# Performance work log

Hardware: AMD Instinct MI355X
Metric: run time of the kernel (lower is better)

The kernel has to match this reference:

```python
import jax, jax.numpy as jnp
import numpy as np

NX = 1024
N_HEAD = 16
B = 2
N = 2048


def setup_inputs() -> dict:
    key = jax.random.key(0)
    k1, k2, k3 = jax.random.split(key, 3)
    x = jax.random.normal(k1, (B, N, NX), dtype=jnp.float32)
    # masked_fill mask: True where attention is NOT allowed (above diagonal)
    mask_self_attention = ~jnp.tril(jnp.ones((N, N), dtype=bool))[None, None]
    c_attn_w = jax.random.normal(k2, (NX, 3 * NX), dtype=jnp.float32) * 0.02
    c_attn_b = jnp.zeros((3 * NX,), dtype=jnp.float32)
    c_proj_w = jax.random.normal(k3, (NX, NX), dtype=jnp.float32) * 0.02
    c_proj_b = jnp.zeros((NX,), dtype=jnp.float32)
    return {
        'x': x,
        'c_attn_w': c_attn_w,
        'c_attn_b': c_attn_b,
        'c_proj_w': c_proj_w,
        'c_proj_b': c_proj_b,
        'mask_self_attention': mask_self_attention,
    }


def reference(x, c_attn_w, c_attn_b, c_proj_w, c_proj_b, mask_self_attention):
    hd = NX // N_HEAD  # head dim = 64
    qkv = x @ c_attn_w + c_attn_b                      # [B,N,3*NX]
    q, k, v = jnp.split(qkv, 3, axis=-1)
    # split heads -> [B,H,N,hd]
    q = q.reshape(B, N, N_HEAD, hd).transpose(0, 2, 1, 3)
    v = v.reshape(B, N, N_HEAD, hd).transpose(0, 2, 1, 3)
    k_t = k.reshape(B, N, N_HEAD, hd).transpose(0, 2, 3, 1)  # [B,H,hd,N]
    present = jnp.stack((k_t.transpose(0, 1, 3, 2), v))      # [2,B,H,N,hd]
    w = jnp.einsum('bhqd,bhdk->bhqk', q, k_t)
    w = w / jnp.sqrt(jnp.float32(hd))  # scale=True
    w = jnp.where(mask_self_attention, jnp.float32(-10000.0), w)
    w = jax.nn.softmax(w, axis=-1)
    a = jnp.einsum('bhqk,bhkd->bhqd', w, v)            # [B,H,N,hd]
    a = a.transpose(0, 2, 1, 3).reshape(B, N, NX)      # merge heads
    a = a @ c_proj_w + c_proj_b
    return (a, present)
```

## Files before the change

kernel.cpp:

```cpp
#include <hip/hip_runtime.h>
#include <cstddef>
#include <cstdint>

#define NX_ 1024
#define NH_ 16
#define HD_ 64
#define B_  2
#define N_  2048
#define M_  (B_ * N_)

typedef __attribute__((ext_vector_type(8))) short bf16x8;
typedef __attribute__((ext_vector_type(4))) float f32x4;

__device__ __forceinline__ unsigned short f2bf(float f) {
    union { float f; unsigned u; } v; v.f = f;
    return (unsigned short)((v.u + 0x7FFFu + ((v.u >> 16) & 1u)) >> 16);
}
__device__ __forceinline__ unsigned pk2bf(float a, float b) {
    return (unsigned)f2bf(a) | ((unsigned)f2bf(b) << 16);
}
__device__ __forceinline__ int szf(int r) { return (r & 3) ^ ((r >> 2) & 3); }

template<int NOUT, int MODE>
__global__ __launch_bounds__(256, 2)
void gemm_mfma(const float* __restrict__ Af, const unsigned short* __restrict__ Ah,
               const float* __restrict__ W, const float* __restrict__ bias,
               float* __restrict__ o_pk, float* __restrict__ o_pv,
               unsigned short* __restrict__ o_q, unsigned short* __restrict__ o_k,
               unsigned short* __restrict__ o_vt, float* __restrict__ o_f)
{
    __shared__ __align__(16) unsigned short As[2][128 * 32];
    __shared__ __align__(16) unsigned short Bs[2][128 * 32];
    const int t = threadIdx.x;
    const int l = t & 63;
    const int g = l >> 4, q15 = l & 15;
    const int w = t >> 6, wm = w >> 1, wn = w & 1;
    const int m0 = blockIdx.y * 128, j0 = blockIdx.x * 128;

    f32x4 acc[4][4];
#pragma unroll
    for (int i = 0; i < 4; i++)
#pragma unroll
        for (int j = 0; j < 4; j++) { acc[i][j][0]=0.f; acc[i][j][1]=0.f; acc[i][j][2]=0.f; acc[i][j][3]=0.f; }

    const int ra = t >> 1, ca = (t & 1) * 16;
    const int nb = t & 127, kb0 = (t >> 7) * 16;

    unsigned sa[8], sb[8];

#define LOAD_A(K0)                                                              \
    do {                                                                        \
        if (MODE == 0) {                                                        \
            const float* ap = Af + (size_t)(m0 + ra) * 1024 + (K0) + ca;        \
            float4 x0 = *(const float4*)(ap);                                   \
            float4 x1 = *(const float4*)(ap + 4);                               \
            float4 x2 = *(const float4*)(ap + 8);                               \
            float4 x3 = *(const float4*)(ap + 12);                              \
            sa[0] = pk2bf(x0.x, x0.y); sa[1] = pk2bf(x0.z, x0.w);               \
            sa[2] = pk2bf(x1.x, x1.y); sa[3] = pk2bf(x1.z, x1.w);               \
            sa[4] = pk2bf(x2.x, x2.y); sa[5] = pk2bf(x2.z, x2.w);               \
            sa[6] = pk2bf(x3.x, x3.y); sa[7] = pk2bf(x3.z, x3.w);               \
        } else {                                                                \
            const uint4* ap = (const uint4*)(Ah + (size_t)(m0 + ra) * 1024 + (K0) + ca); \
            uint4 u0 = ap[0], u1 = ap[1];                                       \
            sa[0]=u0.x; sa[1]=u0.y; sa[2]=u0.z; sa[3]=u0.w;                     \
            sa[4]=u1.x; sa[5]=u1.y; sa[6]=u1.z; sa[7]=u1.w;                     \
        }                                                                       \
    } while (0)

#define LOAD_B(K0)                                                              \
    do {                                                                        \
        const float* wp = W + (size_t)((K0) + kb0) * NOUT + j0 + nb;            \
        float v0,v1;                                                            \
        _Pragma("unroll")                                                       \
        for (int i = 0; i < 8; i++) {                                           \
            v0 = wp[(size_t)(2*i) * NOUT]; v1 = wp[(size_t)(2*i+1) * NOUT];     \
            sb[i] = pk2bf(v0, v1);                                              \
        }                                                                       \
    } while (0)

#define COMMIT_AB(BUF)                                                          \
    do {                                                                        \
        unsigned short* da = &As[BUF][ra * 32];                                 \
        const int s0a = (ca >> 3);                                              \
        *(uint4*)&da[((s0a ^ szf(ra)) & 3) * 8]       = *(uint4*)&sa[0];        \
        *(uint4*)&da[(((s0a + 1) ^ szf(ra)) & 3) * 8] = *(uint4*)&sa[4];        \
        unsigned short* db = &Bs[BUF][nb * 32];                                 \
        const int s0b = (kb0 >> 3);                                             \
        *(uint4*)&db[((s0b ^ szf(nb)) & 3) * 8]       = *(uint4*)&sb[0];        \
        *(uint4*)&db[(((s0b + 1) ^ szf(nb)) & 3) * 8] = *(uint4*)&sb[4];        \
    } while (0)

    LOAD_A(0); LOAD_B(0); COMMIT_AB(0);
    __syncthreads();

    for (int k0 = 0; k0 < 1024; k0 += 32) {
        const int buf = (k0 >> 5) & 1;
        const bool more = (k0 + 32 < 1024);
        if (more) { LOAD_A(k0 + 32); LOAD_B(k0 + 32); }

        bf16x8 af[4], bf[4];
#pragma unroll
        for (int mt = 0; mt < 4; mt++) {
            const int m = wm * 64 + mt * 16 + q15;
            af[mt] = *(const bf16x8*)&As[buf][m * 32 + ((g ^ szf(m)) & 3) * 8];
        }
#pragma unroll
        for (int nt = 0; nt < 4; nt++) {
            const int n = wn * 64 + nt * 16 + q15;
            bf[nt] = *(const bf16x8*)&Bs[buf][n * 32 + ((g ^ szf(n)) & 3) * 8];
        }
#pragma unroll
        for (int mt = 0; mt < 4; mt++)
#pragma unroll
            for (int nt = 0; nt < 4; nt++)
                acc[mt][nt] = __builtin_amdgcn_mfma_f32_16x16x32_bf16(af[mt], bf[nt], acc[mt][nt], 0, 0, 0);

        if (more) COMMIT_AB(buf ^ 1);
        __syncthreads();
    }

#pragma unroll
    for (int nt = 0; nt < 4; nt++) {
        const int ncol = wn * 64 + nt * 16 + q15;
        const int jc = j0 + ncol;
        const float bz = bias[jc];
        const int sec = jc >> 10, jl = jc & 1023, hh = jl >> 6, dd = jl & 63;
#pragma unroll
        for (int mt = 0; mt < 4; mt++) {
#pragma unroll
            for (int r = 0; r < 4; r++) {
                const int m = m0 + wm * 64 + mt * 16 + g * 4 + r;
                const float val = acc[mt][nt][r] + bz;
                if (MODE == 1) {
                    o_f[(size_t)m * NOUT + jc] = val;
                } else {
                    const int bb = m >> 11, nn = m & 2047;
                    const int bhh = bb * NH_ + hh;
                    const size_t idx = ((size_t)bhh * N_ + nn) * HD_ + dd;
                    if (sec == 0)      o_q[idx] = f2bf(val * 0.18033688f);
                    else if (sec == 1) { o_pk[idx] = val; o_k[idx] = f2bf(val); }
                    else               { o_pv[idx] = val;
                                         o_vt[((size_t)bhh * HD_ + dd) * N_ + nn] = f2bf(val); }
                }
            }
        }
    }
#undef LOAD_A
#undef LOAD_B
#undef COMMIT_AB
}

__global__ __launch_bounds__(256, 4)
void attn_mfma(const unsigned short* __restrict__ q_bf,
               const unsigned short* __restrict__ k_bf,
               const unsigned short* __restrict__ v_t,
               unsigned short* __restrict__ a_pre)
{
    __shared__ __align__(16) unsigned short Ks[2][64 * 64];
    __shared__ __align__(16) unsigned short Vt[2][64 * 64];
    __shared__ __align__(16) unsigned short Ps[64 * 64];

    const int t = threadIdx.x, l = t & 63, w = t >> 6;
    const int g = l >> 4, q15 = l & 15;
    const int bh = (int)blockIdx.x & 31;
    const int qt = 31 - ((int)blockIdx.x >> 5);
    const int b = bh >> 4, h = bh & 15;

    const unsigned short* kb  = k_bf + (size_t)bh * N_ * HD_;
    const unsigned short* vtb = v_t  + (size_t)bh * HD_ * N_;

    const int qrow = w * 16 + q15;
    const unsigned short* qp = q_bf + ((size_t)bh * N_ + (size_t)qt * 64 + qrow) * HD_ + g * 8;
    const bf16x8 qf0 = *(const bf16x8*)(qp);
    const bf16x8 qf1 = *(const bf16x8*)(qp + 32);

    const int sr = t >> 2, sc2 = (t & 3) * 2;
    uint4 stgK0, stgK1, stgV0, stgV1;

#define ISSUE(KT)                                                               \
    do {                                                                        \
        const uint4* ksrc = (const uint4*)(kb + ((size_t)((KT) * 64 + sr)) * HD_ + sc2 * 8); \
        stgK0 = ksrc[0]; stgK1 = ksrc[1];                                       \
        const uint4* vsrc = (const uint4*)(vtb + (size_t)sr * N_ + (KT) * 64 + sc2 * 8);     \
        stgV0 = vsrc[0]; stgV1 = vsrc[1];                                       \
    } while (0)

#define COMMIT(BUF)                                                             \
    do {                                                                        \
        unsigned short* kd = &Ks[BUF][sr * 64];                                 \
        *(uint4*)&kd[((sc2 ^ (sr & 7)) & 7) * 8]       = stgK0;                 \
        *(uint4*)&kd[(((sc2 + 1) ^ (sr & 7)) & 7) * 8] = stgK1;                 \
        unsigned short* vd = &Vt[BUF][sr * 64];                                 \
        *(uint4*)&vd[((sc2 ^ (sr & 7)) & 7) * 8]       = stgV0;                 \
        *(uint4*)&vd[(((sc2 + 1) ^ (sr & 7)) & 7) * 8] = stgV1;                 \
    } while (0)

    ISSUE(0); COMMIT(0);
    __syncthreads();

    float m_i = -3.0e38f, l_i = 0.f;
    f32x4 oacc[4];
#pragma unroll
    for (int i = 0; i < 4; i++) { oacc[i][0]=0.f; oacc[i][1]=0.f; oacc[i][2]=0.f; oacc[i][3]=0.f; }

    int cur = 0;
    char* const prow = (char*)Ps + qrow * 128;
    const int psw = (qrow & 7) << 4;

    for (int kt = 0; kt <= qt; kt++) {
        const bool more = (kt < qt);
        if (more) ISSUE(kt + 1);

        f32x4 sacc[4];
#pragma unroll
        for (int i = 0; i < 4; i++) { sacc[i][0]=0.f; sacc[i][1]=0.f; sacc[i][2]=0.f; sacc[i][3]=0.f; }
#pragma unroll
        for (int kt4 = 0; kt4 < 4; kt4++) {
            const int row = kt4 * 16 + q15;
            const bf16x8 kf0 = *(const bf16x8*)&Ks[cur][row * 64 + ((g ^ (row & 7)) & 7) * 8];
            sacc[kt4] = __builtin_amdgcn_mfma_f32_16x16x32_bf16(kf0, qf0, sacc[kt4], 0, 0, 0);
            const bf16x8 kf1 = *(const bf16x8*)&Ks[cur][row * 64 + (((g + 4) ^ (row & 7)) & 7) * 8];
            sacc[kt4] = __builtin_amdgcn_mfma_f32_16x16x32_bf16(kf1, qf1, sacc[kt4], 0, 0, 0);
        }

        float sv[16];
#pragma unroll
        for (int kt4 = 0; kt4 < 4; kt4++)
#pragma unroll
            for (int r = 0; r < 4; r++) sv[kt4 * 4 + r] = sacc[kt4][r];

        if (kt == qt) {
#pragma unroll
            for (int kt4 = 0; kt4 < 4; kt4++)
#pragma unroll
                for (int r = 0; r < 4; r++)
                    if (kt4 * 16 + g * 4 + r > qrow) sv[kt4 * 4 + r] = -3.0e38f;
        }

        float mx = sv[0];
#pragma unroll
        for (int i = 1; i < 16; i++) mx = fmaxf(mx, sv[i]);
        mx = fmaxf(mx, __shfl_xor(mx, 16));
        mx = fmaxf(mx, __shfl_xor(mx, 32));
        const float mnew = fmaxf(m_i, mx);
        const float corr = exp2f(m_i - mnew);
        float ps = 0.f;
#pragma unroll
        for (int i = 0; i < 16; i++) { const float p = exp2f(sv[i] - mnew); sv[i] = p; ps += p; }
        ps += __shfl_xor(ps, 16);
        ps += __shfl_xor(ps, 32);
        l_i = l_i * corr + ps;
        m_i = mnew;
#pragma unroll
        for (int dt = 0; dt < 4; dt++) {
            oacc[dt][0] *= corr; oacc[dt][1] *= corr; oacc[dt][2] *= corr; oacc[dt][3] *= corr;
        }

#pragma unroll
        for (int kt4 = 0; kt4 < 4; kt4++) {
#pragma unroll
            for (int j2 = 0; j2 < 2; j2++) {
                const int kc = kt4 * 16 + g * 4 + j2 * 2;
                *(unsigned*)(prow + ((kc * 2) ^ psw)) = pk2bf(sv[kt4 * 4 + j2 * 2], sv[kt4 * 4 + j2 * 2 + 1]);
            }
        }

        {
            const bf16x8 pf0 = *(const bf16x8*)(prow + ((g * 16) ^ psw));
#pragma unroll
            for (int dt = 0; dt < 4; dt++) {
                const int vrow = dt * 16 + q15;
                const bf16x8 vf = *(const bf16x8*)&Vt[cur][vrow * 64 + ((g ^ (vrow & 7)) & 7) * 8];
                oacc[dt] = __builtin_amdgcn_mfma_f32_16x16x32_bf16(vf, pf0, oacc[dt], 0, 0, 0);
            }
            const bf16x8 pf1 = *(const bf16x8*)(prow + (((g + 4) * 16) ^ psw));
#pragma unroll
            for (int dt = 0; dt < 4; dt++) {
                const int vrow = dt * 16 + q15;
                const bf16x8 vf = *(const bf16x8*)&Vt[cur][vrow * 64 + (((g + 4) ^ (vrow & 7)) & 7) * 8];
                oacc[dt] = __builtin_amdgcn_mfma_f32_16x16x32_bf16(vf, pf1, oacc[dt], 0, 0, 0);
            }
        }

        if (more) COMMIT(cur ^ 1);
        __syncthreads();
        cur ^= 1;
    }

    const float inv = 1.0f / l_i;
    unsigned short* ap2 = a_pre + ((size_t)(b * N_ + qt * 64 + qrow)) * NX_ + h * 64;
#pragma unroll
    for (int dt = 0; dt < 4; dt++) {
#pragma unroll
        for (int j2 = 0; j2 < 2; j2++) {
            const int d = dt * 16 + g * 4 + j2 * 2;
            *(unsigned*)(ap2 + d) = pk2bf(oacc[dt][j2 * 2] * inv, oacc[dt][j2 * 2 + 1] * inv);
        }
    }
#undef ISSUE
#undef COMMIT
}

extern "C" void kernel_launch(void* const* d_in, const int* in_sizes, int n_in,
                              void* d_out, int out_size, void* d_ws, size_t ws_size,
                              hipStream_t stream)
{
    (void)in_sizes; (void)n_in; (void)out_size; (void)ws_size;
    const float* x    = (const float*)d_in[0];
    const float* wqkv = (const float*)d_in[1];
    const float* bqkv = (const float*)d_in[2];
    const float* wpr  = (const float*)d_in[3];
    const float* bpr  = (const float*)d_in[4];

    float* out   = (float*)d_out;
    float* a_out = out;
    float* pk    = out + (size_t)M_ * NX_;
    float* pv    = pk + (size_t)B_ * NH_ * N_ * HD_;

    unsigned short* q_bf  = (unsigned short*)d_ws;
    unsigned short* k_bf  = q_bf + (size_t)B_ * NH_ * N_ * HD_;
    unsigned short* v_t   = k_bf + (size_t)B_ * NH_ * N_ * HD_;
    unsigned short* a_pre = v_t  + (size_t)B_ * NH_ * N_ * HD_;

    gemm_mfma<3 * NX_, 0><<<dim3(24, 32), 256, 0, stream>>>(
        x, nullptr, wqkv, bqkv, pk, pv, q_bf, k_bf, v_t, nullptr);
    attn_mfma<<<dim3(32 * 32), 256, 0, stream>>>(q_bf, k_bf, v_t, a_pre);
    gemm_mfma<NX_, 1><<<dim3(8, 32), 256, 0, stream>>>(
        nullptr, a_pre, wpr, bpr, nullptr, nullptr, nullptr, nullptr, nullptr, a_out);
}
```

Baseline: 244.4 us.

## Pre-convert x and weights to bf16 and stage GEMM tiles via direct global-to-LDS loads

```diff
diff --git a/kernel.cpp b/kernel.cpp
--- a/kernel.cpp
+++ b/kernel.cpp
@@ -19,20 +19,51 @@
 __device__ __forceinline__ unsigned pk2bf(float a, float b) {
     return (unsigned)f2bf(a) | ((unsigned)f2bf(b) << 16);
 }
-__device__ __forceinline__ int szf(int r) { return (r & 3) ^ ((r >> 2) & 3); }
+
+__device__ __forceinline__ void gload_lds16(const void* g, void* l) {
+    __builtin_amdgcn_global_load_lds(
+        (const __attribute__((address_space(1))) unsigned int*)g,
+        (__attribute__((address_space(3))) unsigned int*)l, 16, 0, 0);
+}
+
+__global__ void conv_x(const float* __restrict__ in, unsigned short* __restrict__ outb)
+{
+    const size_t i = ((size_t)blockIdx.x * 256 + threadIdx.x) * 8;
+    const float4 a = *(const float4*)(in + i);
+    const float4 b = *(const float4*)(in + i + 4);
+    uint4 o;
+    o.x = pk2bf(a.x, a.y); o.y = pk2bf(a.z, a.w);
+    o.z = pk2bf(b.x, b.y); o.w = pk2bf(b.z, b.w);
+    *(uint4*)(outb + i) = o;
+}
+
+__global__ void conv_t(const float* __restrict__ W, unsigned short* __restrict__ Wt, int ncols)
+{
+    __shared__ unsigned short tile[32][40];
+    const int t = threadIdx.x;
+    const int n0 = blockIdx.x * 32, k0 = blockIdx.y * 32;
+    const int r = t >> 3, c4 = (t & 7) * 4;
+    const float4 v = *(const float4*)(W + (size_t)(k0 + r) * ncols + n0 + c4);
+    tile[r][c4 + 0] = f2bf(v.x); tile[r][c4 + 1] = f2bf(v.y);
+    tile[r][c4 + 2] = f2bf(v.z); tile[r][c4 + 3] = f2bf(v.w);
+    __syncthreads();
+    uint2 o;
+    o.x = (unsigned)tile[c4 + 0][r] | ((unsigned)tile[c4 + 1][r] << 16);
+    o.y = (unsigned)tile[c4 + 2][r] | ((unsigned)tile[c4 + 3][r] << 16);
+    *(uint2*)(Wt + (size_t)(n0 + r) * 1024 + k0 + c4) = o;
+}
 
 template<int NOUT, int MODE>
-__global__ __launch_bounds__(256, 2)
-void gemm_mfma(const float* __restrict__ Af, const unsigned short* __restrict__ Ah,
-               const float* __restrict__ W, const float* __restrict__ bias,
+__global__ __launch_bounds__(256, 3)
+void gemm_mfma(const unsigned short* __restrict__ Ab, const unsigned short* __restrict__ Wt,
+               const float* __restrict__ bias,
                float* __restrict__ o_pk, float* __restrict__ o_pv,
                unsigned short* __restrict__ o_q, unsigned short* __restrict__ o_k,
                unsigned short* __restrict__ o_vt, float* __restrict__ o_f)
 {
     __shared__ __align__(16) unsigned short As[2][128 * 32];
     __shared__ __align__(16) unsigned short Bs[2][128 * 32];
-    const int t = threadIdx.x;
-    const int l = t & 63;
+    const int t = threadIdx.x, l = t & 63;
     const int g = l >> 4, q15 = l & 15;
     const int w = t >> 6, wm = w >> 1, wn = w & 1;
     const int m0 = blockIdx.y * 128, j0 = blockIdx.x * 128;
@@ -43,72 +74,39 @@
 #pragma unroll
         for (int j = 0; j < 4; j++) { acc[i][j][0]=0.f; acc[i][j][1]=0.f; acc[i][j][2]=0.f; acc[i][j][3]=0.f; }
 
-    const int ra = t >> 1, ca = (t & 1) * 16;
-    const int nb = t & 127, kb0 = (t >> 7) * 16;
-
-    unsigned sa[8], sb[8];
-
-#define LOAD_A(K0)                                                              \
+    const int srow[2] = { (w * 2 + 0) * 16 + (l >> 2), (w * 2 + 1) * 16 + (l >> 2) };
+    const int kct0 = (l & 3) ^ (srow[0] & 3);
+    const int kct1 = (l & 3) ^ (srow[1] & 3);
+
+#define STAGE(BUF, K0)                                                          \
     do {                                                                        \
-        if (MODE == 0) {                                                        \
-            const float* ap = Af + (size_t)(m0 + ra) * 1024 + (K0) + ca;        \
-            float4 x0 = *(const float4*)(ap);                                   \
-            float4 x1 = *(const float4*)(ap + 4);                               \
-            float4 x2 = *(const float4*)(ap + 8);                               \
-            float4 x3 = *(const float4*)(ap + 12);                              \
-            sa[0] = pk2bf(x0.x, x0.y); sa[1] = pk2bf(x0.z, x0.w);               \
-            sa[2] = pk2bf(x1.x, x1.y); sa[3] = pk2bf(x1.z, x1.w);               \
-            sa[4] = pk2bf(x2.x, x2.y); sa[5] = pk2bf(x2.z, x2.w);               \
-            sa[6] = pk2bf(x3.x, x3.y); sa[7] = pk2bf(x3.z, x3.w);               \
-        } else {                                                                \
-            const uint4* ap = (const uint4*)(Ah + (size_t)(m0 + ra) * 1024 + (K0) + ca); \
-            uint4 u0 = ap[0], u1 = ap[1];                                       \
-            sa[0]=u0.x; sa[1]=u0.y; sa[2]=u0.z; sa[3]=u0.w;                     \
-            sa[4]=u1.x; sa[5]=u1.y; sa[6]=u1.z; sa[7]=u1.w;                     \
-        }                                                                       \
+        gload_lds16(Ab + (size_t)(m0 + srow[0]) * 1024 + (K0) + kct0 * 8,       \
+                    &As[BUF][(w * 2 + 0) * 64 * 8]);                            \
+        gload_lds16(Ab + (size_t)(m0 + srow[1]) * 1024 + (K0) + kct1 * 8,       \
+                    &As[BUF][(w * 2 + 1) * 64 * 8]);                            \
+        gload_lds16(Wt + (size_t)(j0 + srow[0]) * 1024 + (K0) + kct0 * 8,       \
+                    &Bs[BUF][(w * 2 + 0) * 64 * 8]);                            \
+        gload_lds16(Wt + (size_t)(j0 + srow[1]) * 1024 + (K0) + kct1 * 8,       \
+                    &Bs[BUF][(w * 2 + 1) * 64 * 8]);                            \
     } while (0)
 
-#define LOAD_B(K0)                                                              \
-    do {                                                                        \
-        const float* wp = W + (size_t)((K0) + kb0) * NOUT + j0 + nb;            \
-        float v0,v1;                                                            \
-        _Pragma("unroll")                                                       \
-        for (int i = 0; i < 8; i++) {                                           \
-            v0 = wp[(size_t)(2*i) * NOUT]; v1 = wp[(size_t)(2*i+1) * NOUT];     \
-            sb[i] = pk2bf(v0, v1);                                              \
-        }                                                                       \
-    } while (0)
-
-#define COMMIT_AB(BUF)                                                          \
-    do {                                                                        \
-        unsigned short* da = &As[BUF][ra * 32];                                 \
-        const int s0a = (ca >> 3);                                              \
-        *(uint4*)&da[((s0a ^ szf(ra)) & 3) * 8]       = *(uint4*)&sa[0];        \
-        *(uint4*)&da[(((s0a + 1) ^ szf(ra)) & 3) * 8] = *(uint4*)&sa[4];        \
-        unsigned short* db = &Bs[BUF][nb * 32];                                 \
-        const int s0b = (kb0 >> 3);                                             \
-        *(uint4*)&db[((s0b ^ szf(nb)) & 3) * 8]       = *(uint4*)&sb[0];        \
-        *(uint4*)&db[(((s0b + 1) ^ szf(nb)) & 3) * 8] = *(uint4*)&sb[4];        \
-    } while (0)
-
-    LOAD_A(0); LOAD_B(0); COMMIT_AB(0);
+    STAGE(0, 0);
     __syncthreads();
 
     for (int k0 = 0; k0 < 1024; k0 += 32) {
         const int buf = (k0 >> 5) & 1;
-        const bool more = (k0 + 32 < 1024);
-        if (more) { LOAD_A(k0 + 32); LOAD_B(k0 + 32); }
+        if (k0 + 32 < 1024) STAGE(buf ^ 1, k0 + 32);
 
         bf16x8 af[4], bf[4];
 #pragma unroll
         for (int mt = 0; mt < 4; mt++) {
             const int m = wm * 64 + mt * 16 + q15;
-            af[mt] = *(const bf16x8*)&As[buf][m * 32 + ((g ^ szf(m)) & 3) * 8];
+            af[mt] = *(const bf16x8*)&As[buf][m * 32 + ((g ^ (m & 3)) & 3) * 8];
         }
 #pragma unroll
         for (int nt = 0; nt < 4; nt++) {
             const int n = wn * 64 + nt * 16 + q15;
-            bf[nt] = *(const bf16x8*)&Bs[buf][n * 32 + ((g ^ szf(n)) & 3) * 8];
+            bf[nt] = *(const bf16x8*)&Bs[buf][n * 32 + ((g ^ (n & 3)) & 3) * 8];
         }
 #pragma unroll
         for (int mt = 0; mt < 4; mt++)
@@ -116,7 +114,6 @@
             for (int nt = 0; nt < 4; nt++)
                 acc[mt][nt] = __builtin_amdgcn_mfma_f32_16x16x32_bf16(af[mt], bf[nt], acc[mt][nt], 0, 0, 0);
 
-        if (more) COMMIT_AB(buf ^ 1);
         __syncthreads();
     }
 
@@ -146,9 +143,7 @@
             }
         }
     }
-#undef LOAD_A
-#undef LOAD_B
-#undef COMMIT_AB
+#undef STAGE
 }
 
 __global__ __launch_bounds__(256, 4)
@@ -318,14 +313,22 @@
     float* pk    = out + (size_t)M_ * NX_;
     float* pv    = pk + (size_t)B_ * NH_ * N_ * HD_;
 
-    unsigned short* q_bf  = (unsigned short*)d_ws;
-    unsigned short* k_bf  = q_bf + (size_t)B_ * NH_ * N_ * HD_;
-    unsigned short* v_t   = k_bf + (size_t)B_ * NH_ * N_ * HD_;
-    unsigned short* a_pre = v_t  + (size_t)B_ * NH_ * N_ * HD_;
+    const size_t SEG = (size_t)M_ * NX_;
+    unsigned short* xb      = (unsigned short*)d_ws;
+    unsigned short* q_bf    = xb + SEG;
+    unsigned short* k_bf    = q_bf + SEG;
+    unsigned short* v_t     = k_bf + SEG;
+    unsigned short* wqkv_t  = v_t + SEG;
+    unsigned short* wproj_t = wqkv_t + (size_t)3 * NX_ * NX_;
+    unsigned short* a_pre   = xb;
+
+    conv_x<<<2048, 256, 0, stream>>>(x, xb);
+    conv_t<<<dim3(96, 32), 256, 0, stream>>>(wqkv, wqkv_t, 3 * NX_);
+    conv_t<<<dim3(32, 32), 256, 0, stream>>>(wpr, wproj_t, NX_);
 
     gemm_mfma<3 * NX_, 0><<<dim3(24, 32), 256, 0, stream>>>(
-        x, nullptr, wqkv, bqkv, pk, pv, q_bf, k_bf, v_t, nullptr);
+        xb, wqkv_t, bqkv, pk, pv, q_bf, k_bf, v_t, nullptr);
     attn_mfma<<<dim3(32 * 32), 256, 0, stream>>>(q_bf, k_bf, v_t, a_pre);
     gemm_mfma<NX_, 1><<<dim3(8, 32), 256, 0, stream>>>(
-        nullptr, a_pre, wpr, bpr, nullptr, nullptr, nullptr, nullptr, nullptr, a_out);
-}
+        a_pre, wproj_t, bpr, nullptr, nullptr, nullptr, nullptr, nullptr, a_out);
+}
```

After: 218.0 us. -10.8%, faster.
